# Performance work log

Measured on AMD Instinct MI355X. Metric: run time of the kernel, lower is better.

## Reference

```python
import jax, jax.numpy as jnp
import numpy as np

NEG_INF = -9e15  # matches the torch module's zero_vec constant
ALPHA = 0.2      # LeakyReLU negative slope


def setup_inputs() -> dict:
    key = jax.random.key(0)
    k1, k2, k3, k4, k5, k6 = jax.random.split(key, 6)
    N_t, N_o, F_in, F_out = 8192, 8192, 256, 64
    return {
        "t_input": jax.random.normal(k1, (N_t, F_in), dtype=jnp.float32),
        "o_input": jax.random.normal(k2, (N_o, F_in), dtype=jnp.float32),
        "W_t": jax.random.normal(k3, (F_in, F_out), dtype=jnp.float32) * 0.1,
        "W_o": jax.random.normal(k4, (F_in, F_out), dtype=jnp.float32) * 0.1,
        "a": jax.random.normal(k5, (2 * F_out, 1), dtype=jnp.float32) * 0.1,
        "adj": jax.random.randint(k6, (N_t, N_o), 0, 2, dtype=jnp.int32),
    }


def reference(t_input, o_input, W_t, W_o, a, adj):
    # Linear projections
    h_t = t_input @ W_t            # [N_t, F]
    h_o = o_input @ W_o            # [N_o, F]
    F_out = h_t.shape[1]
    a_t = a[:F_out, 0]             # [F]
    a_o = a[F_out:, 0]             # [F]
    # e[i,j] = leakyrelu(cat(h_t[i], h_o[j]) . a) = leakyrelu(h_t[i].a_t + h_o[j].a_o)
    # (avoids materializing the N_t*N_o*2F concat tensor; same math)
    e = jax.nn.leaky_relu(
        (h_t @ a_t)[:, None] + (h_o @ a_o)[None, :], negative_slope=ALPHA
    )                              # [N_t, N_o]
    attention = jnp.where(adj > 0, e, NEG_INF)
    attention = jax.nn.softmax(attention, axis=1)
    # dropout is identity at eval time
    h_prime = attention @ h_o      # [N_t, F]
    return jax.nn.elu(h_prime)     # concat=True
```

## Files before the change

### kernel.cpp

```cpp
#include <hip/hip_runtime.h>
#include <math.h>

#define NT 8192
#define NO 8192
#define FIN 256
#define FOUT 64
#define SPLIT 8
#define JSP (NO/SPLIT)
#define ROWT 64

#define OFF_ST  ((size_t)0)
#define OFF_SO  (OFF_ST + (size_t)NT)
#define OFF_WT  (OFF_SO + (size_t)NO)
#define OFF_WO  (OFF_WT + (size_t)FIN)
#define OFF_NUM (OFF_WO + (size_t)FIN)
#define OFF_DEN (OFF_NUM + (size_t)SPLIT*NT*FOUT)
#define OFF_HOB (OFF_DEN + (size_t)SPLIT*NT)

typedef __attribute__((ext_vector_type(8))) short short8;
typedef __attribute__((ext_vector_type(4))) float float4v;

static __device__ __forceinline__ unsigned short f2bf(float x) {
  unsigned int u = __float_as_uint(x);
  unsigned int r = (u + 0x7fffu + ((u >> 16) & 1u)) >> 16;
  return (unsigned short)r;
}
static __device__ __forceinline__ int pk2(float a, float b) {
  return (int)((unsigned int)f2bf(a) | ((unsigned int)f2bf(b) << 16));
}
static __device__ __forceinline__ float bflo(int p) {
  return __uint_as_float(((unsigned int)p) << 16);
}
static __device__ __forceinline__ float bfhi(int p) {
  return __uint_as_float(((unsigned int)p) & 0xffff0000u);
}

__global__ void k_wvec(const float* __restrict__ Wt, const float* __restrict__ Wo,
                       const float* __restrict__ a, float* __restrict__ ws) {
  int k = threadIdx.x;
  float s1 = 0.f, s2 = 0.f;
#pragma unroll
  for (int fq = 0; fq < FOUT/4; ++fq) {
    float4 wt4 = *(const float4*)(Wt + (size_t)k*FOUT + fq*4);
    float4 wo4 = *(const float4*)(Wo + (size_t)k*FOUT + fq*4);
    float4 at4 = *(const float4*)(a + fq*4);
    float4 ao4 = *(const float4*)(a + FOUT + fq*4);
    s1 += wt4.x*at4.x + wt4.y*at4.y + wt4.z*at4.z + wt4.w*at4.w;
    s2 += wo4.x*ao4.x + wo4.y*ao4.y + wo4.z*ao4.z + wo4.w*ao4.w;
  }
  ws[OFF_WT + k] = s1;
  ws[OFF_WO + k] = s2;
}

__global__ void k_st(const float* __restrict__ tin, float* __restrict__ ws) {
  int lane = threadIdx.x & 63;
  int wv   = threadIdx.x >> 6;
  int row  = blockIdx.x * 4 + wv;
  float4 v = ((const float4*)(tin + (size_t)row*FIN))[lane];
  float4 w = ((const float4*)(ws + OFF_WT))[lane];
  float p = v.x*w.x + v.y*w.y + v.z*w.z + v.w*w.w;
#pragma unroll
  for (int m = 32; m >= 1; m >>= 1) p += __shfl_xor(p, m, 64);
  if (lane == 0) ws[OFF_ST + row] = p;
}

__global__ void k_ho(const float* __restrict__ oin, const float* __restrict__ Wo,
                     const float* __restrict__ a, float* __restrict__ ws) {
  unsigned short* hob = (unsigned short*)(ws + OFF_HOB);
  int lane = threadIdx.x & 63;
  int wv = __builtin_amdgcn_readfirstlane(threadIdx.x >> 6);
  int r0 = blockIdx.x * 32 + wv * 8;
  const float* ob = oin + (size_t)r0 * FIN;
  float acc[8];
#pragma unroll
  for (int r = 0; r < 8; ++r) acc[r] = 0.f;
#pragma unroll 2
  for (int k = 0; k < FIN; k += 4) {
    float w0 = Wo[(size_t)(k+0)*FOUT + lane];
    float w1 = Wo[(size_t)(k+1)*FOUT + lane];
    float w2 = Wo[(size_t)(k+2)*FOUT + lane];
    float w3 = Wo[(size_t)(k+3)*FOUT + lane];
#pragma unroll
    for (int r = 0; r < 8; ++r) {
      float4 ov = *(const float4*)(ob + (size_t)r*FIN + k);
      acc[r] = fmaf(ov.x, w0, acc[r]);
      acc[r] = fmaf(ov.y, w1, acc[r]);
      acc[r] = fmaf(ov.z, w2, acc[r]);
      acc[r] = fmaf(ov.w, w3, acc[r]);
    }
  }
  float ao = a[FOUT + lane];
#pragma unroll
  for (int r = 0; r < 8; ++r) {
    hob[(size_t)lane*NO + r0 + r] = f2bf(acc[r]);
    float p = acc[r] * ao;
#pragma unroll
    for (int m = 32; m >= 1; m >>= 1) p += __shfl_xor(p, m, 64);
    if (lane == 0) ws[OFF_SO + r0 + r] = p;
  }
}

__launch_bounds__(256, 4)
__global__ void k_attn(const int* __restrict__ adj, float* __restrict__ ws) {
  const float* st = ws + OFF_ST;
  const float* so = ws + OFF_SO;
  const unsigned short* hob = (const unsigned short*)(ws + OFF_HOB);
  float* gnum = ws + OFF_NUM;
  float* gden = ws + OFF_DEN;

  int t = threadIdx.x;
  int wv = t >> 6, lane = t & 63;
  int bx = blockIdx.x;
  int s  = bx & (SPLIT - 1);
  int bi = bx >> 3;
  int i0 = bi * ROWT;
  int jb = s * JSP;

  int r16 = lane & 15;
  int kg  = lane >> 4;
  int irow = i0 + wv*16 + r16;

  float sti = st[irow];

  const int* ap            = adj + (size_t)irow*NO + jb + kg*8;
  const float* sop         = so + jb + kg*8;
  const unsigned short* hp = hob + (size_t)r16*NO + jb + kg*8;

  float4v acc0 = (float4v)0.f, acc1 = (float4v)0.f;
  float4v acc2 = (float4v)0.f, acc3 = (float4v)0.f;
  float dsum = 0.f;

#pragma unroll 1
  for (int tt = 0; tt < JSP/32; ++tt) {
    int off = tt*32;
    int4   a0 = *(const int4*)(ap + off);
    int4   a1 = *(const int4*)(ap + off + 4);
    float4 s0 = *(const float4*)(sop + off);
    float4 s1 = *(const float4*)(sop + off + 4);
    short8 b0 = *(const short8*)(hp + off);
    short8 b1 = *(const short8*)(hp + (size_t)16*NO + off);
    short8 b2 = *(const short8*)(hp + (size_t)32*NO + off);
    short8 b3 = *(const short8*)(hp + (size_t)48*NO + off);

    float x0 = sti + s0.x; x0 = fmaxf(x0, 0.2f*x0);
    float x1 = sti + s0.y; x1 = fmaxf(x1, 0.2f*x1);
    float x2 = sti + s0.z; x2 = fmaxf(x2, 0.2f*x2);
    float x3 = sti + s0.w; x3 = fmaxf(x3, 0.2f*x3);
    float x4 = sti + s1.x; x4 = fmaxf(x4, 0.2f*x4);
    float x5 = sti + s1.y; x5 = fmaxf(x5, 0.2f*x5);
    float x6 = sti + s1.z; x6 = fmaxf(x6, 0.2f*x6);
    float x7 = sti + s1.w; x7 = fmaxf(x7, 0.2f*x7);
    float w0 = (a0.x > 0) ? __expf(x0) : 0.f;
    float w1 = (a0.y > 0) ? __expf(x1) : 0.f;
    float w2 = (a0.z > 0) ? __expf(x2) : 0.f;
    float w3 = (a0.w > 0) ? __expf(x3) : 0.f;
    float w4 = (a1.x > 0) ? __expf(x4) : 0.f;
    float w5 = (a1.y > 0) ? __expf(x5) : 0.f;
    float w6 = (a1.z > 0) ? __expf(x6) : 0.f;
    float w7 = (a1.w > 0) ? __expf(x7) : 0.f;

    int p01 = pk2(w0, w1);
    int p23 = pk2(w2, w3);
    int p45 = pk2(w4, w5);
    int p67 = pk2(w6, w7);
    dsum += bflo(p01) + bfhi(p01) + bflo(p23) + bfhi(p23)
          + bflo(p45) + bfhi(p45) + bflo(p67) + bfhi(p67);

    int4 ai = {p01, p23, p45, p67};
    short8 afrag = *(short8*)&ai;

    acc0 = __builtin_amdgcn_mfma_f32_16x16x32_bf16(afrag, b0, acc0, 0, 0, 0);
    acc1 = __builtin_amdgcn_mfma_f32_16x16x32_bf16(afrag, b1, acc1, 0, 0, 0);
    acc2 = __builtin_amdgcn_mfma_f32_16x16x32_bf16(afrag, b2, acc2, 0, 0, 0);
    acc3 = __builtin_amdgcn_mfma_f32_16x16x32_bf16(afrag, b3, acc3, 0, 0, 0);
  }

  dsum += __shfl_xor(dsum, 16, 64);
  dsum += __shfl_xor(dsum, 32, 64);
  if (lane < 16) gden[(size_t)s*NT + i0 + wv*16 + lane] = dsum;

  float4v accs[4] = {acc0, acc1, acc2, acc3};
#pragma unroll
  for (int g = 0; g < 4; ++g)
#pragma unroll
    for (int r = 0; r < 4; ++r) {
      int i = i0 + wv*16 + kg*4 + r;
      int f = g*16 + r16;
      gnum[((size_t)s*NT + i)*FOUT + f] = accs[g][r];
    }
}

__global__ void k_comb(const float* __restrict__ ws, float* __restrict__ out) {
  int idx = blockIdx.x * 256 + threadIdx.x;
  int i = idx >> 6;
  float num = 0.f, den = 0.f;
#pragma unroll
  for (int s = 0; s < SPLIT; ++s) {
    num += ws[OFF_NUM + ((size_t)s*NT + i)*FOUT + (idx & 63)];
    den += ws[OFF_DEN + (size_t)s*NT + i];
  }
  float r = num / den;
  out[idx] = (r > 0.f) ? r : (__expf(r) - 1.f);
}

extern "C" void kernel_launch(void* const* d_in, const int* in_sizes, int n_in,
                              void* d_out, int out_size, void* d_ws, size_t ws_size,
                              hipStream_t stream) {
  const float* tin = (const float*)d_in[0];
  const float* oin = (const float*)d_in[1];
  const float* Wt  = (const float*)d_in[2];
  const float* Wo  = (const float*)d_in[3];
  const float* a   = (const float*)d_in[4];
  const int*   adj = (const int*)d_in[5];
  float* out = (float*)d_out;
  float* ws  = (float*)d_ws;

  hipLaunchKernelGGL(k_wvec, dim3(1),              dim3(256), 0, stream, Wt, Wo, a, ws);
  hipLaunchKernelGGL(k_st,   dim3(NT/4),           dim3(256), 0, stream, tin, ws);
  hipLaunchKernelGGL(k_ho,   dim3(NO/32),          dim3(256), 0, stream, oin, Wo, a, ws);
  hipLaunchKernelGGL(k_attn, dim3(NT/ROWT*SPLIT),  dim3(256), 0, stream, adj, ws);
  hipLaunchKernelGGL(k_comb, dim3(NT*FOUT/256),    dim3(256), 0, stream, ws, out);
}
```

Before: 463.3 us.

## Precompute adjacency bitmask and factorized exp table, relayout h_o for MFMA

A new pre-pass packs the int32 adjacency matrix into a bitmask, so the attention kernel streams 32x less mask data. It also factorizes exp(leakyrelu(st+so)) into per-row and per-column exponentials, stored as a table of exp(so) and exp(0.2*so), which removes the per-element transcendental from the inner loop. The bf16 h_o matrix is rewritten in an MFMA-fragment-tiled layout so B-operand loads are contiguous. Row weights are redistributed across lanes with ds_bpermute. The cost is an extra full pass over adj and two extra launches, plus possible overflow or precision changes from multiplying exponentials separately.

```diff
diff --git a/kernel.cpp b/kernel.cpp
--- a/kernel.cpp
+++ b/kernel.cpp
@@ -8,6 +8,7 @@
 #define SPLIT 8
 #define JSP (NO/SPLIT)
 #define ROWT 64
+#define NW32 (NO/32)
 
 #define OFF_ST  ((size_t)0)
 #define OFF_SO  (OFF_ST + (size_t)NT)
@@ -16,6 +17,8 @@
 #define OFF_NUM (OFF_WO + (size_t)FIN)
 #define OFF_DEN (OFF_NUM + (size_t)SPLIT*NT*FOUT)
 #define OFF_HOB (OFF_DEN + (size_t)SPLIT*NT)
+#define OFF_ETA (OFF_HOB + (size_t)NO*FOUT/2)
+#define OFF_MSK (OFF_ETA + (size_t)NO*2)
 
 typedef __attribute__((ext_vector_type(8))) short short8;
 typedef __attribute__((ext_vector_type(4))) float float4v;
@@ -33,6 +36,24 @@
 }
 static __device__ __forceinline__ float bfhi(int p) {
   return __uint_as_float(((unsigned int)p) & 0xffff0000u);
+}
+
+__global__ void k_mask(const int* __restrict__ adj, float* __restrict__ ws) {
+  unsigned int* mw = (unsigned int*)(ws + OFF_MSK);
+  int wv = threadIdx.x >> 6, lane = threadIdx.x & 63;
+  int gw = blockIdx.x * 4 + wv;
+  const int NCH = NT*NO/256;
+#pragma unroll 2
+  for (int c = gw; c < NCH; c += 8192) {
+    int4 a = *(const int4*)(adj + (size_t)c*256 + lane*4);
+    unsigned int nib = (a.x > 0 ? 1u : 0u) | (a.y > 0 ? 2u : 0u)
+                     | (a.z > 0 ? 4u : 0u) | (a.w > 0 ? 8u : 0u);
+    unsigned int val = nib << ((lane & 7) * 4);
+    val |= __shfl_xor((int)val, 1, 64);
+    val |= __shfl_xor((int)val, 2, 64);
+    val |= __shfl_xor((int)val, 4, 64);
+    if ((lane & 7) == 0) mw[(size_t)c*8 + (lane >> 3)] = val;
+  }
 }
 
 __global__ void k_wvec(const float* __restrict__ Wt, const float* __restrict__ Wo,
@@ -66,14 +87,14 @@
 
 __global__ void k_ho(const float* __restrict__ oin, const float* __restrict__ Wo,
                      const float* __restrict__ a, float* __restrict__ ws) {
-  unsigned short* hob = (unsigned short*)(ws + OFF_HOB);
+  unsigned short* hobp = (unsigned short*)(ws + OFF_HOB);
   int lane = threadIdx.x & 63;
   int wv = __builtin_amdgcn_readfirstlane(threadIdx.x >> 6);
-  int r0 = blockIdx.x * 32 + wv * 8;
+  int r0 = blockIdx.x * 16 + wv * 4;
   const float* ob = oin + (size_t)r0 * FIN;
-  float acc[8];
-#pragma unroll
-  for (int r = 0; r < 8; ++r) acc[r] = 0.f;
+  float acc[4];
+#pragma unroll
+  for (int r = 0; r < 4; ++r) acc[r] = 0.f;
 #pragma unroll 2
   for (int k = 0; k < FIN; k += 4) {
     float w0 = Wo[(size_t)(k+0)*FOUT + lane];
@@ -81,7 +102,7 @@
     float w2 = Wo[(size_t)(k+2)*FOUT + lane];
     float w3 = Wo[(size_t)(k+3)*FOUT + lane];
 #pragma unroll
-    for (int r = 0; r < 8; ++r) {
+    for (int r = 0; r < 4; ++r) {
       float4 ov = *(const float4*)(ob + (size_t)r*FIN + k);
       acc[r] = fmaf(ov.x, w0, acc[r]);
       acc[r] = fmaf(ov.y, w1, acc[r]);
@@ -90,21 +111,34 @@
     }
   }
   float ao = a[FOUT + lane];
-#pragma unroll
-  for (int r = 0; r < 8; ++r) {
-    hob[(size_t)lane*NO + r0 + r] = f2bf(acc[r]);
+  int fg = lane >> 4, n16 = lane & 15;
+#pragma unroll
+  for (int r = 0; r < 4; ++r) {
+    int j = r0 + r;
+    int jt = j >> 5, jl = j & 31;
+    int ldst = (jl >> 3) * 16 + n16;
+    int e = jl & 7;
+    hobp[(((size_t)jt*4 + fg)*64 + ldst)*8 + e] = f2bf(acc[r]);
     float p = acc[r] * ao;
 #pragma unroll
     for (int m = 32; m >= 1; m >>= 1) p += __shfl_xor(p, m, 64);
-    if (lane == 0) ws[OFF_SO + r0 + r] = p;
-  }
+    if (lane == 0) ws[OFF_SO + j] = p;
+  }
+}
+
+__global__ void k_etab(float* __restrict__ ws) {
+  int j = blockIdx.x * 256 + threadIdx.x;
+  float s = ws[OFF_SO + j];
+  ws[OFF_ETA + 2*j + 0] = __expf(s);
+  ws[OFF_ETA + 2*j + 1] = __expf(0.2f * s);
 }
 
 __launch_bounds__(256, 4)
-__global__ void k_attn(const int* __restrict__ adj, float* __restrict__ ws) {
+__global__ void k_attn(float* __restrict__ ws) {
   const float* st = ws + OFF_ST;
-  const float* so = ws + OFF_SO;
-  const unsigned short* hob = (const unsigned short*)(ws + OFF_HOB);
+  const float* etab = ws + OFF_ETA;
+  const unsigned int* maskw = (const unsigned int*)(ws + OFF_MSK);
+  const unsigned short* hobp = (const unsigned short*)(ws + OFF_HOB);
   float* gnum = ws + OFF_NUM;
   float* gden = ws + OFF_DEN;
 
@@ -116,15 +150,19 @@
   int i0 = bi * ROWT;
   int jb = s * JSP;
 
-  int r16 = lane & 15;
-  int kg  = lane >> 4;
-  int irow = i0 + wv*16 + r16;
-
-  float sti = st[irow];
-
-  const int* ap            = adj + (size_t)irow*NO + jb + kg*8;
-  const float* sop         = so + jb + kg*8;
-  const unsigned short* hp = hob + (size_t)r16*NO + jb + kg*8;
+  int rsrc = lane >> 2, csrc = lane & 3;
+  int irow_s = i0 + wv*16 + rsrc;
+  float sti  = st[irow_s];
+  float esti  = __expf(sti);
+  float esti2 = __expf(0.2f * sti);
+  float ethr  = __expf(-sti);
+
+  const unsigned int* mrow = maskw + (size_t)irow_s * NW32 + (jb >> 5);
+  const float* ep = etab + (size_t)(jb + csrc*8) * 2;
+  const unsigned short* hpb = hobp + (size_t)(jb >> 5) * 2048 + lane*8;
+
+  int r16 = lane & 15, kg = lane >> 4;
+  int sidx4 = ((r16 * 4 + kg) << 2);
 
   float4v acc0 = (float4v)0.f, acc1 = (float4v)0.f;
   float4v acc2 = (float4v)0.f, acc3 = (float4v)0.f;
@@ -132,41 +170,40 @@
 
 #pragma unroll 1
   for (int tt = 0; tt < JSP/32; ++tt) {
-    int off = tt*32;
-    int4   a0 = *(const int4*)(ap + off);
-    int4   a1 = *(const int4*)(ap + off + 4);
-    float4 s0 = *(const float4*)(sop + off);
-    float4 s1 = *(const float4*)(sop + off + 4);
-    short8 b0 = *(const short8*)(hp + off);
-    short8 b1 = *(const short8*)(hp + (size_t)16*NO + off);
-    short8 b2 = *(const short8*)(hp + (size_t)32*NO + off);
-    short8 b3 = *(const short8*)(hp + (size_t)48*NO + off);
-
-    float x0 = sti + s0.x; x0 = fmaxf(x0, 0.2f*x0);
-    float x1 = sti + s0.y; x1 = fmaxf(x1, 0.2f*x1);
-    float x2 = sti + s0.z; x2 = fmaxf(x2, 0.2f*x2);
-    float x3 = sti + s0.w; x3 = fmaxf(x3, 0.2f*x3);
-    float x4 = sti + s1.x; x4 = fmaxf(x4, 0.2f*x4);
-    float x5 = sti + s1.y; x5 = fmaxf(x5, 0.2f*x5);
-    float x6 = sti + s1.z; x6 = fmaxf(x6, 0.2f*x6);
-    float x7 = sti + s1.w; x7 = fmaxf(x7, 0.2f*x7);
-    float w0 = (a0.x > 0) ? __expf(x0) : 0.f;
-    float w1 = (a0.y > 0) ? __expf(x1) : 0.f;
-    float w2 = (a0.z > 0) ? __expf(x2) : 0.f;
-    float w3 = (a0.w > 0) ? __expf(x3) : 0.f;
-    float w4 = (a1.x > 0) ? __expf(x4) : 0.f;
-    float w5 = (a1.y > 0) ? __expf(x5) : 0.f;
-    float w6 = (a1.z > 0) ? __expf(x6) : 0.f;
-    float w7 = (a1.w > 0) ? __expf(x7) : 0.f;
-
-    int p01 = pk2(w0, w1);
-    int p23 = pk2(w2, w3);
-    int p45 = pk2(w4, w5);
-    int p67 = pk2(w6, w7);
-    dsum += bflo(p01) + bfhi(p01) + bflo(p23) + bfhi(p23)
-          + bflo(p45) + bfhi(p45) + bflo(p67) + bfhi(p67);
-
-    int4 ai = {p01, p23, p45, p67};
+    unsigned int mwv = mrow[tt];
+    const float* e_ = ep + tt*64;
+    float4 e0 = *(const float4*)(e_);
+    float4 e1 = *(const float4*)(e_ + 4);
+    float4 e2 = *(const float4*)(e_ + 8);
+    float4 e3 = *(const float4*)(e_ + 12);
+    const unsigned short* hb = hpb + (size_t)tt*2048;
+    short8 b0 = *(const short8*)(hb);
+    short8 b1 = *(const short8*)(hb + 512);
+    short8 b2 = *(const short8*)(hb + 1024);
+    short8 b3 = *(const short8*)(hb + 1536);
+
+    unsigned int msh = mwv >> (csrc * 8);
+    float w0 = ((e0.x >= ethr) ? esti*e0.x : esti2*e0.y); w0 = (msh & 1u)   ? w0 : 0.f;
+    float w1 = ((e0.z >= ethr) ? esti*e0.z : esti2*e0.w); w1 = (msh & 2u)   ? w1 : 0.f;
+    float w2 = ((e1.x >= ethr) ? esti*e1.x : esti2*e1.y); w2 = (msh & 4u)   ? w2 : 0.f;
+    float w3 = ((e1.z >= ethr) ? esti*e1.z : esti2*e1.w); w3 = (msh & 8u)   ? w3 : 0.f;
+    float w4 = ((e2.x >= ethr) ? esti*e2.x : esti2*e2.y); w4 = (msh & 16u)  ? w4 : 0.f;
+    float w5 = ((e2.z >= ethr) ? esti*e2.z : esti2*e2.w); w5 = (msh & 32u)  ? w5 : 0.f;
+    float w6 = ((e3.x >= ethr) ? esti*e3.x : esti2*e3.y); w6 = (msh & 64u)  ? w6 : 0.f;
+    float w7 = ((e3.z >= ethr) ? esti*e3.z : esti2*e3.w); w7 = (msh & 128u) ? w7 : 0.f;
+
+    int p0 = pk2(w0, w1);
+    int p1 = pk2(w2, w3);
+    int p2 = pk2(w4, w5);
+    int p3 = pk2(w6, w7);
+    dsum += bflo(p0) + bfhi(p0) + bflo(p1) + bfhi(p1)
+          + bflo(p2) + bfhi(p2) + bflo(p3) + bfhi(p3);
+
+    int4 ai;
+    ai.x = __builtin_amdgcn_ds_bpermute(sidx4, p0);
+    ai.y = __builtin_amdgcn_ds_bpermute(sidx4, p1);
+    ai.z = __builtin_amdgcn_ds_bpermute(sidx4, p2);
+    ai.w = __builtin_amdgcn_ds_bpermute(sidx4, p3);
     short8 afrag = *(short8*)&ai;
 
     acc0 = __builtin_amdgcn_mfma_f32_16x16x32_bf16(afrag, b0, acc0, 0, 0, 0);
@@ -175,19 +212,18 @@
     acc3 = __builtin_amdgcn_mfma_f32_16x16x32_bf16(afrag, b3, acc3, 0, 0, 0);
   }
 
-  dsum += __shfl_xor(dsum, 16, 64);
-  dsum += __shfl_xor(dsum, 32, 64);
-  if (lane < 16) gden[(size_t)s*NT + i0 + wv*16 + lane] = dsum;
-
-  float4v accs[4] = {acc0, acc1, acc2, acc3};
-#pragma unroll
-  for (int g = 0; g < 4; ++g)
-#pragma unroll
-    for (int r = 0; r < 4; ++r) {
-      int i = i0 + wv*16 + kg*4 + r;
-      int f = g*16 + r16;
-      gnum[((size_t)s*NT + i)*FOUT + f] = accs[g][r];
-    }
+  dsum += __shfl_xor(dsum, 1, 64);
+  dsum += __shfl_xor(dsum, 2, 64);
+  if (csrc == 0) gden[(size_t)s*NT + i0 + wv*16 + rsrc] = dsum;
+
+  size_t obase = ((size_t)s*NT + i0 + wv*16 + kg*4) * FOUT + r16;
+#pragma unroll
+  for (int r = 0; r < 4; ++r) {
+    gnum[obase + (size_t)r*FOUT +  0] = acc0[r];
+    gnum[obase + (size_t)r*FOUT + 16] = acc1[r];
+    gnum[obase + (size_t)r*FOUT + 32] = acc2[r];
+    gnum[obase + (size_t)r*FOUT + 48] = acc3[r];
+  }
 }
 
 __global__ void k_comb(const float* __restrict__ ws, float* __restrict__ out) {
@@ -215,9 +251,11 @@
   float* out = (float*)d_out;
   float* ws  = (float*)d_ws;
 
+  hipLaunchKernelGGL(k_mask, dim3(2048),           dim3(256), 0, stream, adj, ws);
   hipLaunchKernelGGL(k_wvec, dim3(1),              dim3(256), 0, stream, Wt, Wo, a, ws);
   hipLaunchKernelGGL(k_st,   dim3(NT/4),           dim3(256), 0, stream, tin, ws);
-  hipLaunchKernelGGL(k_ho,   dim3(NO/32),          dim3(256), 0, stream, oin, Wo, a, ws);
-  hipLaunchKernelGGL(k_attn, dim3(NT/ROWT*SPLIT),  dim3(256), 0, stream, adj, ws);
+  hipLaunchKernelGGL(k_ho,   dim3(NO/16),          dim3(256), 0, stream, oin, Wo, a, ws);
+  hipLaunchKernelGGL(k_etab, dim3(NO/256),         dim3(256), 0, stream, ws);
+  hipLaunchKernelGGL(k_attn, dim3(NT/ROWT*SPLIT),  dim3(256), 0, stream, ws);
   hipLaunchKernelGGL(k_comb, dim3(NT*FOUT/256),    dim3(256), 0, stream, ws, out);
 }
```

Result: no change. 460.6 us (-0.6%).
